# Optimization experiments

Measured on AMD Instinct MI355X. Metric: run time of the kernel, lower is better.

## Reference

```python
import jax, jax.numpy as jnp
import numpy as np

B, S, D, H = 2, 48, 256, 8
DH = D // H  # depth per head = 32
N = S * S    # flattened pair sequence length = 2304


def setup_inputs() -> dict:
    key = jax.random.key(0)
    ks = jax.random.split(key, 9)
    std = 1.0 / np.sqrt(D)
    x = jax.random.normal(ks[0], (B, S, S, D), dtype=jnp.float32)
    Wq = jax.random.normal(ks[1], (D, D), dtype=jnp.float32) * std
    Wk = jax.random.normal(ks[2], (D, D), dtype=jnp.float32) * std
    Wv = jax.random.normal(ks[3], (D, D), dtype=jnp.float32) * std
    Wo = jax.random.normal(ks[4], (D, D), dtype=jnp.float32) * std
    bq = jnp.zeros((D,), jnp.float32)
    bk = jnp.zeros((D,), jnp.float32)
    bv = jnp.zeros((D,), jnp.float32)
    bo = jnp.zeros((D,), jnp.float32)
    return {"pair_representation": x, "Wq": Wq, "bq": bq, "Wk": Wk, "bk": bk,
            "Wv": Wv, "bv": bv, "Wo": Wo, "bo": bo}


def reference(pair_representation, Wq, bq, Wk, bk, Wv, bv, Wo, bo):
    x = pair_representation.reshape(B, N, D)  # flatten (S,S) -> N

    def heads(t):  # (B,N,D) -> (B,H,N,DH)
        return t.reshape(B, N, H, DH).transpose(0, 2, 1, 3)

    q = heads(x @ Wq + bq)
    k = heads(x @ Wk + bk)
    v = heads(x @ Wv + bv)

    scale = 1.0 / jnp.sqrt(jnp.asarray(DH, jnp.float32))
    logits = jnp.einsum('bhnd,bhmd->bhnm', q, k) * scale  # (B,H,N,N)
    attn = jax.nn.softmax(logits, axis=-1)
    ctx = jnp.einsum('bhnm,bhmd->bhnd', attn, v)
    ctx = ctx.transpose(0, 2, 1, 3).reshape(B, N, D)
    return ctx @ Wo + bo  # (B, N, D)
```

## Files before the change

### kernel.cpp

```cpp
#include <hip/hip_runtime.h>
#include <math.h>

#define B 2
#define S 48
#define D 256
#define H 8
#define DH 32
#define N (S*S)
#define BN (B*N)
#define BH (B*H)
#define KS 6
#define KPZ (N/KS)
#define NE ((size_t)BN*D)
#define BHN (BH*N)

typedef _Float16 half8 __attribute__((ext_vector_type(8)));
typedef _Float16 half4_t __attribute__((ext_vector_type(4)));
typedef unsigned short ushort8_t __attribute__((ext_vector_type(8)));
typedef float floatx4 __attribute__((ext_vector_type(4)));

__device__ __forceinline__ void split8(const float* v, half8* hi, half8* lo) {
    #pragma unroll
    for (int j = 0; j < 8; j++) {
        _Float16 h = (_Float16)v[j];
        (*hi)[j] = h;
        (*lo)[j] = (_Float16)(v[j] - (float)h);
    }
}

__global__ __launch_bounds__(256) void proj_kernel(
    const float* __restrict__ x,
    const float* __restrict__ Wq, const float* __restrict__ bq,
    const float* __restrict__ Wk, const float* __restrict__ bk,
    const float* __restrict__ Wv, const float* __restrict__ bv,
    _Float16* __restrict__ qbuf, _Float16* __restrict__ kbuf,
    _Float16* __restrict__ vtbuf)
{
    __shared__ __align__(16) _Float16 BhS[64 * 72];
    __shared__ __align__(16) _Float16 BlS[64 * 72];

    const int z = blockIdx.z;
    const float* W    = (z == 0) ? Wq : (z == 1) ? Wk : Wv;
    const float* bias = (z == 0) ? bq : (z == 1) ? bk : bv;
    const float scale = (z == 0) ? rsqrtf((float)DH) * 1.44269504f : 1.0f;

    const int t = threadIdx.x;
    const int wv2 = t >> 6, lane = t & 63, l15 = lane & 15, quad = lane >> 4;
    const int rowb = blockIdx.x * 64;
    const int colb = blockIdx.y * 64;
    const int grow = rowb + wv2 * 16 + l15;
    floatx4 acc[4] = {{0,0,0,0},{0,0,0,0},{0,0,0,0},{0,0,0,0}};

    for (int kb0 = 0; kb0 < D; kb0 += 64) {
        __syncthreads();
        #pragma unroll
        for (int i = 0; i < 2; i++) {
            int u = i * 256 + t;
            int cc = u & 63, k0 = (u >> 6) * 8;
            float v[8];
            #pragma unroll
            for (int j = 0; j < 8; j++)
                v[j] = W[(size_t)(kb0 + k0 + j) * D + colb + cc];
            half8 hi, lo;
            split8(v, &hi, &lo);
            *(half8*)(BhS + cc * 72 + k0) = hi;
            *(half8*)(BlS + cc * 72 + k0) = lo;
        }
        __syncthreads();
        #pragma unroll
        for (int ksx = 0; ksx < 2; ksx++) {
            const float* xp = x + (size_t)grow * D + kb0 + ksx * 32 + quad * 8;
            float4 x0 = *(const float4*)xp;
            float4 x1 = *(const float4*)(xp + 4);
            float v[8] = {x0.x, x0.y, x0.z, x0.w, x1.x, x1.y, x1.z, x1.w};
            half8 ah, al;
            split8(v, &ah, &al);
            #pragma unroll
            for (int cg = 0; cg < 4; cg++) {
                half8 bh8 = *(const half8*)(BhS + (cg * 16 + l15) * 72 + ksx * 32 + quad * 8);
                half8 bl8 = *(const half8*)(BlS + (cg * 16 + l15) * 72 + ksx * 32 + quad * 8);
                acc[cg] = __builtin_amdgcn_mfma_f32_16x16x32_f16(ah, bh8, acc[cg], 0, 0, 0);
                acc[cg] = __builtin_amdgcn_mfma_f32_16x16x32_f16(al, bh8, acc[cg], 0, 0, 0);
                acc[cg] = __builtin_amdgcn_mfma_f32_16x16x32_f16(ah, bl8, acc[cg], 0, 0, 0);
            }
        }
    }

    const int bb = (rowb >= N) ? 1 : 0;
    #pragma unroll
    for (int cg = 0; cg < 4; cg++) {
        int col = colb + cg * 16 + l15;
        int hh = col >> 5, dh = col & 31;
        float bs = bias[col];
        if (z < 2) {
            _Float16* op = (z == 0) ? qbuf : kbuf;
            #pragma unroll
            for (int r = 0; r < 4; r++) {
                int n = rowb + wv2 * 16 + quad * 4 + r - bb * N;
                float v = (acc[cg][r] + bs) * scale;
                op[((size_t)(bb * H + hh) * N + n) * DH + dh] = (_Float16)v;
            }
        } else {
            int n0 = rowb + wv2 * 16 + quad * 4 - bb * N;
            half4_t pk;
            #pragma unroll
            for (int r = 0; r < 4; r++) pk[r] = (_Float16)(acc[cg][r] + bs);
            *(half4_t*)(vtbuf + ((size_t)(bb * H + hh) * DH + dh) * N + n0) = pk;
        }
    }
}

__global__ __launch_bounds__(256) void attn_kernel(
    const _Float16* __restrict__ qbuf, const _Float16* __restrict__ kbuf,
    const _Float16* __restrict__ vtbuf,
    _Float16* __restrict__ ctx_part, float* __restrict__ lpart)
{
    __shared__ __align__(16) _Float16 Ks[64 * 40];
    __shared__ __align__(16) _Float16 Vt[32 * 72];

    const int t = threadIdx.x;
    const int wv2 = t >> 6, lane = t & 63, l15 = lane & 15, quad = lane >> 4;
    const int bh = blockIdx.y, kz = blockIdx.z;
    const int qbase = blockIdx.x * 128 + wv2 * 32;

    half8 bq8[2];
    #pragma unroll
    for (int qg = 0; qg < 2; qg++)
        bq8[qg] = *(const half8*)(qbuf +
            ((size_t)bh * N + qbase + qg * 16 + l15) * DH + quad * 8);

    floatx4 acc[2][2] = {{{0,0,0,0},{0,0,0,0}},{{0,0,0,0},{0,0,0,0}}};
    float lsum[2] = {0.f, 0.f};

    const int skey = t >> 2, sd0 = (t & 3) * 8;
    const int svd = t >> 3, svk = (t & 7) * 8;

    for (int it = 0; it < KPZ / 64; it++) {
        const int key0 = kz * KPZ + it * 64;
        __syncthreads();
        *(ushort8_t*)(Ks + skey * 40 + sd0) =
            *(const ushort8_t*)(kbuf + ((size_t)bh * N + key0 + skey) * DH + sd0);
        *(ushort8_t*)(Vt + svd * 72 + svk) =
            *(const ushort8_t*)(vtbuf + ((size_t)bh * DH + svd) * N + key0 + svk);
        __syncthreads();

        #pragma unroll
        for (int kg = 0; kg < 4; kg++) {
            half8 ka = *(const half8*)(Ks + (kg * 16 + l15) * 40 + quad * 8);
            half4_t va0 = *(const half4_t*)(Vt + l15 * 72 + kg * 16 + quad * 4);
            half4_t va1 = *(const half4_t*)(Vt + (16 + l15) * 72 + kg * 16 + quad * 4);
            #pragma unroll
            for (int qg = 0; qg < 2; qg++) {
                floatx4 s = {0, 0, 0, 0};
                s = __builtin_amdgcn_mfma_f32_16x16x32_f16(ka, bq8[qg], s, 0, 0, 0);
                half4_t pf;
                #pragma unroll
                for (int r = 0; r < 4; r++) {
                    float p = exp2f(s[r]);
                    lsum[qg] += p;
                    pf[r] = (_Float16)p;
                }
                acc[qg][0] = __builtin_amdgcn_mfma_f32_16x16x16f16(va0, pf, acc[qg][0], 0, 0, 0);
                acc[qg][1] = __builtin_amdgcn_mfma_f32_16x16x16f16(va1, pf, acc[qg][1], 0, 0, 0);
            }
        }
    }

    const int bb = bh >> 3, hh = bh & 7;
    #pragma unroll
    for (int qg = 0; qg < 2; qg++) {
        float ls = lsum[qg];
        ls += __shfl_xor(ls, 16);
        ls += __shfl_xor(ls, 32);
        int q = qbase + qg * 16 + l15;
        if (quad == 0) lpart[(size_t)kz * BHN + bh * N + q] = ls;
        _Float16* crow = ctx_part + (size_t)kz * NE + ((size_t)bb * N + q) * D + hh * DH;
        half4_t c0, c1;
        #pragma unroll
        for (int r = 0; r < 4; r++) {
            c0[r] = (_Float16)acc[qg][0][r];
            c1[r] = (_Float16)acc[qg][1][r];
        }
        *(half4_t*)(crow + quad * 4)      = c0;
        *(half4_t*)(crow + 16 + quad * 4) = c1;
    }
}

__global__ __launch_bounds__(256) void outproj_kernel(
    const _Float16* __restrict__ ctx_part, const float* __restrict__ lpart,
    const float* __restrict__ Wo, const float* __restrict__ bo,
    float* __restrict__ out)
{
    __shared__ __align__(16) _Float16 BhS[64 * 72];
    __shared__ __align__(16) _Float16 BlS[64 * 72];
    __shared__ float Linv[64 * 8];

    const int t = threadIdx.x;
    const int wv2 = t >> 6, lane = t & 63, l15 = lane & 15, quad = lane >> 4;
    const int rowb = blockIdx.x * 64;
    const int colb = blockIdx.y * 64;
    const int grow = rowb + wv2 * 16 + l15;

    #pragma unroll
    for (int i = 0; i < 2; i++) {
        int idx = i * 256 + t;
        int r = idx >> 3, hh = idx & 7;
        int row = rowb + r;
        int bb = (row >= N) ? 1 : 0;
        int bhn = (bb * H + hh) * N + (row - bb * N);
        float ls = 0.f;
        #pragma unroll
        for (int zz = 0; zz < KS; zz++) ls += lpart[(size_t)zz * BHN + bhn];
        Linv[idx] = 1.0f / ls;
    }

    floatx4 acc[4] = {{0,0,0,0},{0,0,0,0},{0,0,0,0},{0,0,0,0}};

    for (int kb0 = 0; kb0 < D; kb0 += 64) {
        __syncthreads();
        #pragma unroll
        for (int i = 0; i < 2; i++) {
            int u = i * 256 + t;
            int cc = u & 63, k0 = (u >> 6) * 8;
            float v[8];
            #pragma unroll
            for (int j = 0; j < 8; j++)
                v[j] = Wo[(size_t)(kb0 + k0 + j) * D + colb + cc];
            half8 hi, lo;
            split8(v, &hi, &lo);
            *(half8*)(BhS + cc * 72 + k0) = hi;
            *(half8*)(BlS + cc * 72 + k0) = lo;
        }
        __syncthreads();
        #pragma unroll
        for (int ksx = 0; ksx < 2; ksx++) {
            const int kcol = kb0 + ksx * 32 + quad * 8;
            float linv = Linv[(wv2 * 16 + l15) * 8 + (kcol >> 5)];
            float v[8] = {};
            #pragma unroll
            for (int zz = 0; zz < KS; zz++) {
                half8 h = *(const half8*)(ctx_part + (size_t)zz * NE + (size_t)grow * D + kcol);
                #pragma unroll
                for (int j = 0; j < 8; j++) v[j] += (float)h[j];
            }
            #pragma unroll
            for (int j = 0; j < 8; j++) v[j] *= linv;
            half8 ah, al;
            split8(v, &ah, &al);
            #pragma unroll
            for (int cg = 0; cg < 4; cg++) {
                half8 bh8 = *(const half8*)(BhS + (cg * 16 + l15) * 72 + ksx * 32 + quad * 8);
                half8 bl8 = *(const half8*)(BlS + (cg * 16 + l15) * 72 + ksx * 32 + quad * 8);
                acc[cg] = __builtin_amdgcn_mfma_f32_16x16x32_f16(ah, bh8, acc[cg], 0, 0, 0);
                acc[cg] = __builtin_amdgcn_mfma_f32_16x16x32_f16(al, bh8, acc[cg], 0, 0, 0);
                acc[cg] = __builtin_amdgcn_mfma_f32_16x16x32_f16(ah, bl8, acc[cg], 0, 0, 0);
            }
        }
    }

    #pragma unroll
    for (int cg = 0; cg < 4; cg++) {
        int col = colb + cg * 16 + l15;
        float bs = bo[col];
        #pragma unroll
        for (int r = 0; r < 4; r++) {
            int row = rowb + wv2 * 16 + quad * 4 + r;
            out[(size_t)row * D + col] = acc[cg][r] + bs;
        }
    }
}

extern "C" void kernel_launch(void* const* d_in, const int* in_sizes, int n_in,
                              void* d_out, int out_size, void* d_ws, size_t ws_size,
                              hipStream_t stream)
{
    const float* x  = (const float*)d_in[0];
    const float* Wq = (const float*)d_in[1];
    const float* bq = (const float*)d_in[2];
    const float* Wk = (const float*)d_in[3];
    const float* bk = (const float*)d_in[4];
    const float* Wv = (const float*)d_in[5];
    const float* bv = (const float*)d_in[6];
    const float* Wo = (const float*)d_in[7];
    const float* bo = (const float*)d_in[8];
    float* out = (float*)d_out;

    _Float16* ctx_part = (_Float16*)d_ws;
    float* lpart    = (float*)(ctx_part + (size_t)KS * NE);
    _Float16* qbuf  = (_Float16*)(lpart + (size_t)KS * BHN);
    _Float16* kbuf  = qbuf + NE;
    _Float16* vtbuf = kbuf + NE;

    proj_kernel<<<dim3(BN / 64, D / 64, 3), 256, 0, stream>>>(
        x, Wq, bq, Wk, bk, Wv, bv, qbuf, kbuf, vtbuf);

    attn_kernel<<<dim3(N / 128, BH, KS), 256, 0, stream>>>(
        qbuf, kbuf, vtbuf, ctx_part, lpart);

    outproj_kernel<<<dim3(BN / 64, D / 64), 256, 0, stream>>>(
        ctx_part, lpart, Wo, bo, out);
}
```

Measured before the change: 133.9 us.

## Fuse projection, attention and output projection into one persistent kernel with grid barriers

Replaces three kernel launches with a single persistent kernel of 432 blocks that loops over the work items of each phase and separates phases with atomic-counter grid barriers. The aim is to remove launch overhead and inter-kernel gaps. In exchange it adds a memset, barrier spin costs, and a possible deadlock if all 432 blocks are not co-resident. The attention phase now runs fewer concurrent blocks than the original 1728-block grid, and the output phase uses only 288 of the blocks.

```diff
diff --git a/kernel.cpp b/kernel.cpp
--- a/kernel.cpp
+++ b/kernel.cpp
@@ -13,6 +13,7 @@
 #define KPZ (N/KS)
 #define NE ((size_t)BN*D)
 #define BHN (BH*N)
+#define GRID 432
 
 typedef _Float16 half8 __attribute__((ext_vector_type(8)));
 typedef _Float16 half4_t __attribute__((ext_vector_type(4)));
@@ -28,244 +29,256 @@
     }
 }
 
-__global__ __launch_bounds__(256) void proj_kernel(
+__device__ __forceinline__ void grid_barrier(unsigned* cnt) {
+    __threadfence();
+    __syncthreads();
+    if (threadIdx.x == 0) {
+        __hip_atomic_fetch_add(cnt, 1u, __ATOMIC_ACQ_REL, __HIP_MEMORY_SCOPE_AGENT);
+        long guard = 0;
+        while (__hip_atomic_load(cnt, __ATOMIC_ACQUIRE, __HIP_MEMORY_SCOPE_AGENT) < GRID
+               && ++guard < (1L << 31)) { }
+    }
+    __syncthreads();
+    __threadfence();
+}
+
+__global__ __launch_bounds__(256, 2) void fused_kernel(
     const float* __restrict__ x,
     const float* __restrict__ Wq, const float* __restrict__ bq,
     const float* __restrict__ Wk, const float* __restrict__ bk,
     const float* __restrict__ Wv, const float* __restrict__ bv,
+    const float* __restrict__ Wo, const float* __restrict__ bo,
+    float* __restrict__ out,
+    unsigned* __restrict__ counters,
+    _Float16* __restrict__ ctx_part, float* __restrict__ lpart,
     _Float16* __restrict__ qbuf, _Float16* __restrict__ kbuf,
     _Float16* __restrict__ vtbuf)
 {
-    __shared__ __align__(16) _Float16 BhS[64 * 72];
-    __shared__ __align__(16) _Float16 BlS[64 * 72];
-
-    const int z = blockIdx.z;
-    const float* W    = (z == 0) ? Wq : (z == 1) ? Wk : Wv;
-    const float* bias = (z == 0) ? bq : (z == 1) ? bk : bv;
-    const float scale = (z == 0) ? rsqrtf((float)DH) * 1.44269504f : 1.0f;
+    __shared__ __align__(16) unsigned char smem[20480];
 
     const int t = threadIdx.x;
+    const int bid = blockIdx.x;
     const int wv2 = t >> 6, lane = t & 63, l15 = lane & 15, quad = lane >> 4;
-    const int rowb = blockIdx.x * 64;
-    const int colb = blockIdx.y * 64;
-    const int grow = rowb + wv2 * 16 + l15;
-    floatx4 acc[4] = {{0,0,0,0},{0,0,0,0},{0,0,0,0},{0,0,0,0}};
-
-    for (int kb0 = 0; kb0 < D; kb0 += 64) {
-        __syncthreads();
+
+    {
+        _Float16* BhS = (_Float16*)smem;
+        _Float16* BlS = BhS + 64 * 72;
+        for (int u = bid; u < 864; u += GRID) {
+            const int z = u / 288, rem = u % 288;
+            const int rowb = (rem >> 2) * 64, colb = (rem & 3) * 64;
+            const float* W    = (z == 0) ? Wq : (z == 1) ? Wk : Wv;
+            const float* bias = (z == 0) ? bq : (z == 1) ? bk : bv;
+            const float scale = (z == 0) ? rsqrtf((float)DH) * 1.44269504f : 1.0f;
+            const int grow = rowb + wv2 * 16 + l15;
+            floatx4 acc[4] = {{0,0,0,0},{0,0,0,0},{0,0,0,0},{0,0,0,0}};
+
+            for (int kb0 = 0; kb0 < D; kb0 += 64) {
+                __syncthreads();
+                #pragma unroll
+                for (int i = 0; i < 2; i++) {
+                    int uu = i * 256 + t;
+                    int cc = uu & 63, k0 = (uu >> 6) * 8;
+                    float v[8];
+                    #pragma unroll
+                    for (int j = 0; j < 8; j++)
+                        v[j] = W[(size_t)(kb0 + k0 + j) * D + colb + cc];
+                    half8 hi, lo;
+                    split8(v, &hi, &lo);
+                    *(half8*)(BhS + cc * 72 + k0) = hi;
+                    *(half8*)(BlS + cc * 72 + k0) = lo;
+                }
+                __syncthreads();
+                #pragma unroll
+                for (int ksx = 0; ksx < 2; ksx++) {
+                    const float* xp = x + (size_t)grow * D + kb0 + ksx * 32 + quad * 8;
+                    float4 x0 = *(const float4*)xp;
+                    float4 x1 = *(const float4*)(xp + 4);
+                    float v[8] = {x0.x, x0.y, x0.z, x0.w, x1.x, x1.y, x1.z, x1.w};
+                    half8 ah, al;
+                    split8(v, &ah, &al);
+                    #pragma unroll
+                    for (int cg = 0; cg < 4; cg++) {
+                        half8 bh8 = *(const half8*)(BhS + (cg * 16 + l15) * 72 + ksx * 32 + quad * 8);
+                        half8 bl8 = *(const half8*)(BlS + (cg * 16 + l15) * 72 + ksx * 32 + quad * 8);
+                        acc[cg] = __builtin_amdgcn_mfma_f32_16x16x32_f16(ah, bh8, acc[cg], 0, 0, 0);
+                        acc[cg] = __builtin_amdgcn_mfma_f32_16x16x32_f16(al, bh8, acc[cg], 0, 0, 0);
+                        acc[cg] = __builtin_amdgcn_mfma_f32_16x16x32_f16(ah, bl8, acc[cg], 0, 0, 0);
+                    }
+                }
+            }
+
+            const int bb = (rowb >= N) ? 1 : 0;
+            #pragma unroll
+            for (int cg = 0; cg < 4; cg++) {
+                int col = colb + cg * 16 + l15;
+                int hh = col >> 5, dh = col & 31;
+                float bs = bias[col];
+                if (z < 2) {
+                    _Float16* op = (z == 0) ? qbuf : kbuf;
+                    #pragma unroll
+                    for (int r = 0; r < 4; r++) {
+                        int n = rowb + wv2 * 16 + quad * 4 + r - bb * N;
+                        float v = (acc[cg][r] + bs) * scale;
+                        op[((size_t)(bb * H + hh) * N + n) * DH + dh] = (_Float16)v;
+                    }
+                } else {
+                    int n0 = rowb + wv2 * 16 + quad * 4 - bb * N;
+                    half4_t pk;
+                    #pragma unroll
+                    for (int r = 0; r < 4; r++) pk[r] = (_Float16)(acc[cg][r] + bs);
+                    *(half4_t*)(vtbuf + ((size_t)(bb * H + hh) * DH + dh) * N + n0) = pk;
+                }
+            }
+        }
+    }
+    grid_barrier(&counters[0]);
+
+    {
+        _Float16* Ks = (_Float16*)smem;
+        _Float16* Vt = Ks + 64 * 40;
+        const int skey = t >> 2, sd0 = (t & 3) * 8;
+        const int svd = t >> 3, svk = (t & 7) * 8;
+
+        for (int u = bid; u < 1728; u += GRID) {
+            const int xq = u / 96, rem = u % 96;
+            const int bh = rem / 6, kz = rem % 6;
+            const int qbase = xq * 128 + wv2 * 32;
+
+            half8 bq8[2];
+            #pragma unroll
+            for (int qg = 0; qg < 2; qg++)
+                bq8[qg] = *(const half8*)(qbuf +
+                    ((size_t)bh * N + qbase + qg * 16 + l15) * DH + quad * 8);
+
+            floatx4 acc[2][2] = {{{0,0,0,0},{0,0,0,0}},{{0,0,0,0},{0,0,0,0}}};
+            float lsum[2] = {0.f, 0.f};
+
+            for (int it = 0; it < KPZ / 64; it++) {
+                const int key0 = kz * KPZ + it * 64;
+                __syncthreads();
+                *(ushort8_t*)(Ks + skey * 40 + sd0) =
+                    *(const ushort8_t*)(kbuf + ((size_t)bh * N + key0 + skey) * DH + sd0);
+                *(ushort8_t*)(Vt + svd * 72 + svk) =
+                    *(const ushort8_t*)(vtbuf + ((size_t)bh * DH + svd) * N + key0 + svk);
+                __syncthreads();
+
+                #pragma unroll
+                for (int kg = 0; kg < 4; kg++) {
+                    half8 ka = *(const half8*)(Ks + (kg * 16 + l15) * 40 + quad * 8);
+                    half4_t va0 = *(const half4_t*)(Vt + l15 * 72 + kg * 16 + quad * 4);
+                    half4_t va1 = *(const half4_t*)(Vt + (16 + l15) * 72 + kg * 16 + quad * 4);
+                    #pragma unroll
+                    for (int qg = 0; qg < 2; qg++) {
+                        floatx4 s = {0, 0, 0, 0};
+                        s = __builtin_amdgcn_mfma_f32_16x16x32_f16(ka, bq8[qg], s, 0, 0, 0);
+                        half4_t pf;
+                        #pragma unroll
+                        for (int r = 0; r < 4; r++) {
+                            float p = exp2f(s[r]);
+                            lsum[qg] += p;
+                            pf[r] = (_Float16)p;
+                        }
+                        acc[qg][0] = __builtin_amdgcn_mfma_f32_16x16x16f16(va0, pf, acc[qg][0], 0, 0, 0);
+                        acc[qg][1] = __builtin_amdgcn_mfma_f32_16x16x16f16(va1, pf, acc[qg][1], 0, 0, 0);
+                    }
+                }
+            }
+
+            const int bb = bh >> 3, hh = bh & 7;
+            #pragma unroll
+            for (int qg = 0; qg < 2; qg++) {
+                float ls = lsum[qg];
+                ls += __shfl_xor(ls, 16);
+                ls += __shfl_xor(ls, 32);
+                int q = qbase + qg * 16 + l15;
+                if (quad == 0) lpart[(size_t)kz * BHN + bh * N + q] = ls;
+                _Float16* crow = ctx_part + (size_t)kz * NE + ((size_t)bb * N + q) * D + hh * DH;
+                half4_t c0, c1;
+                #pragma unroll
+                for (int r = 0; r < 4; r++) {
+                    c0[r] = (_Float16)acc[qg][0][r];
+                    c1[r] = (_Float16)acc[qg][1][r];
+                }
+                *(half4_t*)(crow + quad * 4)      = c0;
+                *(half4_t*)(crow + 16 + quad * 4) = c1;
+            }
+        }
+    }
+    grid_barrier(&counters[1]);
+
+    if (bid < 288) {
+        _Float16* BhS = (_Float16*)smem;
+        _Float16* BlS = BhS + 64 * 72;
+        float* Linv = (float*)(smem + 18432);
+        const int rowb = (bid >> 2) * 64, colb = (bid & 3) * 64;
+        const int grow = rowb + wv2 * 16 + l15;
+
         #pragma unroll
         for (int i = 0; i < 2; i++) {
-            int u = i * 256 + t;
-            int cc = u & 63, k0 = (u >> 6) * 8;
-            float v[8];
-            #pragma unroll
-            for (int j = 0; j < 8; j++)
-                v[j] = W[(size_t)(kb0 + k0 + j) * D + colb + cc];
-            half8 hi, lo;
-            split8(v, &hi, &lo);
-            *(half8*)(BhS + cc * 72 + k0) = hi;
-            *(half8*)(BlS + cc * 72 + k0) = lo;
-        }
-        __syncthreads();
+            int idx = i * 256 + t;
+            int r = idx >> 3, hh = idx & 7;
+            int row = rowb + r;
+            int bb = (row >= N) ? 1 : 0;
+            int bhn = (bb * H + hh) * N + (row - bb * N);
+            float ls = 0.f;
+            #pragma unroll
+            for (int zz = 0; zz < KS; zz++) ls += lpart[(size_t)zz * BHN + bhn];
+            Linv[idx] = 1.0f / ls;
+        }
+
+        floatx4 acc[4] = {{0,0,0,0},{0,0,0,0},{0,0,0,0},{0,0,0,0}};
+
+        for (int kb0 = 0; kb0 < D; kb0 += 64) {
+            __syncthreads();
+            #pragma unroll
+            for (int i = 0; i < 2; i++) {
+                int uu = i * 256 + t;
+                int cc = uu & 63, k0 = (uu >> 6) * 8;
+                float v[8];
+                #pragma unroll
+                for (int j = 0; j < 8; j++)
+                    v[j] = Wo[(size_t)(kb0 + k0 + j) * D + colb + cc];
+                half8 hi, lo;
+                split8(v, &hi, &lo);
+                *(half8*)(BhS + cc * 72 + k0) = hi;
+                *(half8*)(BlS + cc * 72 + k0) = lo;
+            }
+            __syncthreads();
+            #pragma unroll
+            for (int ksx = 0; ksx < 2; ksx++) {
+                const int kcol = kb0 + ksx * 32 + quad * 8;
+                float linv = Linv[(wv2 * 16 + l15) * 8 + (kcol >> 5)];
+                float v[8] = {};
+                #pragma unroll
+                for (int zz = 0; zz < KS; zz++) {
+                    half8 h = *(const half8*)(ctx_part + (size_t)zz * NE + (size_t)grow * D + kcol);
+                    #pragma unroll
+                    for (int j = 0; j < 8; j++) v[j] += (float)h[j];
+                }
+                #pragma unroll
+                for (int j = 0; j < 8; j++) v[j] *= linv;
+                half8 ah, al;
+                split8(v, &ah, &al);
+                #pragma unroll
+                for (int cg = 0; cg < 4; cg++) {
+                    half8 bh8 = *(const half8*)(BhS + (cg * 16 + l15) * 72 + ksx * 32 + quad * 8);
+                    half8 bl8 = *(const half8*)(BlS + (cg * 16 + l15) * 72 + ksx * 32 + quad * 8);
+                    acc[cg] = __builtin_amdgcn_mfma_f32_16x16x32_f16(ah, bh8, acc[cg], 0, 0, 0);
+                    acc[cg] = __builtin_amdgcn_mfma_f32_16x16x32_f16(al, bh8, acc[cg], 0, 0, 0);
+                    acc[cg] = __builtin_amdgcn_mfma_f32_16x16x32_f16(ah, bl8, acc[cg], 0, 0, 0);
+                }
+            }
+        }
+
         #pragma unroll
-        for (int ksx = 0; ksx < 2; ksx++) {
-            const float* xp = x + (size_t)grow * D + kb0 + ksx * 32 + quad * 8;
-            float4 x0 = *(const float4*)xp;
-            float4 x1 = *(const float4*)(xp + 4);
-            float v[8] = {x0.x, x0.y, x0.z, x0.w, x1.x, x1.y, x1.z, x1.w};
-            half8 ah, al;
-            split8(v, &ah, &al);
-            #pragma unroll
-            for (int cg = 0; cg < 4; cg++) {
-                half8 bh8 = *(const half8*)(BhS + (cg * 16 + l15) * 72 + ksx * 32 + quad * 8);
-                half8 bl8 = *(const half8*)(BlS + (cg * 16 + l15) * 72 + ksx * 32 + quad * 8);
-                acc[cg] = __builtin_amdgcn_mfma_f32_16x16x32_f16(ah, bh8, acc[cg], 0, 0, 0);
-                acc[cg] = __builtin_amdgcn_mfma_f32_16x16x32_f16(al, bh8, acc[cg], 0, 0, 0);
-                acc[cg] = __builtin_amdgcn_mfma_f32_16x16x32_f16(ah, bl8, acc[cg], 0, 0, 0);
-            }
-        }
-    }
-
-    const int bb = (rowb >= N) ? 1 : 0;
-    #pragma unroll
-    for (int cg = 0; cg < 4; cg++) {
-        int col = colb + cg * 16 + l15;
-        int hh = col >> 5, dh = col & 31;
-        float bs = bias[col];
-        if (z < 2) {
-            _Float16* op = (z == 0) ? qbuf : kbuf;
+        for (int cg = 0; cg < 4; cg++) {
+            int col = colb + cg * 16 + l15;
+            float bs = bo[col];
             #pragma unroll
             for (int r = 0; r < 4; r++) {
-                int n = rowb + wv2 * 16 + quad * 4 + r - bb * N;
-                float v = (acc[cg][r] + bs) * scale;
-                op[((size_t)(bb * H + hh) * N + n) * DH + dh] = (_Float16)v;
-            }
-        } else {
-            int n0 = rowb + wv2 * 16 + quad * 4 - bb * N;
-            half4_t pk;
-            #pragma unroll
-            for (int r = 0; r < 4; r++) pk[r] = (_Float16)(acc[cg][r] + bs);
-            *(half4_t*)(vtbuf + ((size_t)(bb * H + hh) * DH + dh) * N + n0) = pk;
-        }
-    }
-}
-
-__global__ __launch_bounds__(256) void attn_kernel(
-    const _Float16* __restrict__ qbuf, const _Float16* __restrict__ kbuf,
-    const _Float16* __restrict__ vtbuf,
-    _Float16* __restrict__ ctx_part, float* __restrict__ lpart)
-{
-    __shared__ __align__(16) _Float16 Ks[64 * 40];
-    __shared__ __align__(16) _Float16 Vt[32 * 72];
-
-    const int t = threadIdx.x;
-    const int wv2 = t >> 6, lane = t & 63, l15 = lane & 15, quad = lane >> 4;
-    const int bh = blockIdx.y, kz = blockIdx.z;
-    const int qbase = blockIdx.x * 128 + wv2 * 32;
-
-    half8 bq8[2];
-    #pragma unroll
-    for (int qg = 0; qg < 2; qg++)
-        bq8[qg] = *(const half8*)(qbuf +
-            ((size_t)bh * N + qbase + qg * 16 + l15) * DH + quad * 8);
-
-    floatx4 acc[2][2] = {{{0,0,0,0},{0,0,0,0}},{{0,0,0,0},{0,0,0,0}}};
-    float lsum[2] = {0.f, 0.f};
-
-    const int skey = t >> 2, sd0 = (t & 3) * 8;
-    const int svd = t >> 3, svk = (t & 7) * 8;
-
-    for (int it = 0; it < KPZ / 64; it++) {
-        const int key0 = kz * KPZ + it * 64;
-        __syncthreads();
-        *(ushort8_t*)(Ks + skey * 40 + sd0) =
-            *(const ushort8_t*)(kbuf + ((size_t)bh * N + key0 + skey) * DH + sd0);
-        *(ushort8_t*)(Vt + svd * 72 + svk) =
-            *(const ushort8_t*)(vtbuf + ((size_t)bh * DH + svd) * N + key0 + svk);
-        __syncthreads();
-
-        #pragma unroll
-        for (int kg = 0; kg < 4; kg++) {
-            half8 ka = *(const half8*)(Ks + (kg * 16 + l15) * 40 + quad * 8);
-            half4_t va0 = *(const half4_t*)(Vt + l15 * 72 + kg * 16 + quad * 4);
-            half4_t va1 = *(const half4_t*)(Vt + (16 + l15) * 72 + kg * 16 + quad * 4);
-            #pragma unroll
-            for (int qg = 0; qg < 2; qg++) {
-                floatx4 s = {0, 0, 0, 0};
-                s = __builtin_amdgcn_mfma_f32_16x16x32_f16(ka, bq8[qg], s, 0, 0, 0);
-                half4_t pf;
-                #pragma unroll
-                for (int r = 0; r < 4; r++) {
-                    float p = exp2f(s[r]);
-                    lsum[qg] += p;
-                    pf[r] = (_Float16)p;
-                }
-                acc[qg][0] = __builtin_amdgcn_mfma_f32_16x16x16f16(va0, pf, acc[qg][0], 0, 0, 0);
-                acc[qg][1] = __builtin_amdgcn_mfma_f32_16x16x16f16(va1, pf, acc[qg][1], 0, 0, 0);
-            }
-        }
-    }
-
-    const int bb = bh >> 3, hh = bh & 7;
-    #pragma unroll
-    for (int qg = 0; qg < 2; qg++) {
-        float ls = lsum[qg];
-        ls += __shfl_xor(ls, 16);
-        ls += __shfl_xor(ls, 32);
-        int q = qbase + qg * 16 + l15;
-        if (quad == 0) lpart[(size_t)kz * BHN + bh * N + q] = ls;
-        _Float16* crow = ctx_part + (size_t)kz * NE + ((size_t)bb * N + q) * D + hh * DH;
-        half4_t c0, c1;
-        #pragma unroll
-        for (int r = 0; r < 4; r++) {
-            c0[r] = (_Float16)acc[qg][0][r];
-            c1[r] = (_Float16)acc[qg][1][r];
-        }
-        *(half4_t*)(crow + quad * 4)      = c0;
-        *(half4_t*)(crow + 16 + quad * 4) = c1;
-    }
-}
-
-__global__ __launch_bounds__(256) void outproj_kernel(
-    const _Float16* __restrict__ ctx_part, const float* __restrict__ lpart,
-    const float* __restrict__ Wo, const float* __restrict__ bo,
-    float* __restrict__ out)
-{
-    __shared__ __align__(16) _Float16 BhS[64 * 72];
-    __shared__ __align__(16) _Float16 BlS[64 * 72];
-    __shared__ float Linv[64 * 8];
-
-    const int t = threadIdx.x;
-    const int wv2 = t >> 6, lane = t & 63, l15 = lane & 15, quad = lane >> 4;
-    const int rowb = blockIdx.x * 64;
-    const int colb = blockIdx.y * 64;
-    const int grow = rowb + wv2 * 16 + l15;
-
-    #pragma unroll
-    for (int i = 0; i < 2; i++) {
-        int idx = i * 256 + t;
-        int r = idx >> 3, hh = idx & 7;
-        int row = rowb + r;
-        int bb = (row >= N) ? 1 : 0;
-        int bhn = (bb * H + hh) * N + (row - bb * N);
-        float ls = 0.f;
-        #pragma unroll
-        for (int zz = 0; zz < KS; zz++) ls += lpart[(size_t)zz * BHN + bhn];
-        Linv[idx] = 1.0f / ls;
-    }
-
-    floatx4 acc[4] = {{0,0,0,0},{0,0,0,0},{0,0,0,0},{0,0,0,0}};
-
-    for (int kb0 = 0; kb0 < D; kb0 += 64) {
-        __syncthreads();
-        #pragma unroll
-        for (int i = 0; i < 2; i++) {
-            int u = i * 256 + t;
-            int cc = u & 63, k0 = (u >> 6) * 8;
-            float v[8];
-            #pragma unroll
-            for (int j = 0; j < 8; j++)
-                v[j] = Wo[(size_t)(kb0 + k0 + j) * D + colb + cc];
-            half8 hi, lo;
-            split8(v, &hi, &lo);
-            *(half8*)(BhS + cc * 72 + k0) = hi;
-            *(half8*)(BlS + cc * 72 + k0) = lo;
-        }
-        __syncthreads();
-        #pragma unroll
-        for (int ksx = 0; ksx < 2; ksx++) {
-            const int kcol = kb0 + ksx * 32 + quad * 8;
-            float linv = Linv[(wv2 * 16 + l15) * 8 + (kcol >> 5)];
-            float v[8] = {};
-            #pragma unroll
-            for (int zz = 0; zz < KS; zz++) {
-                half8 h = *(const half8*)(ctx_part + (size_t)zz * NE + (size_t)grow * D + kcol);
-                #pragma unroll
-                for (int j = 0; j < 8; j++) v[j] += (float)h[j];
-            }
-            #pragma unroll
-            for (int j = 0; j < 8; j++) v[j] *= linv;
-            half8 ah, al;
-            split8(v, &ah, &al);
-            #pragma unroll
-            for (int cg = 0; cg < 4; cg++) {
-                half8 bh8 = *(const half8*)(BhS + (cg * 16 + l15) * 72 + ksx * 32 + quad * 8);
-                half8 bl8 = *(const half8*)(BlS + (cg * 16 + l15) * 72 + ksx * 32 + quad * 8);
-                acc[cg] = __builtin_amdgcn_mfma_f32_16x16x32_f16(ah, bh8, acc[cg], 0, 0, 0);
-                acc[cg] = __builtin_amdgcn_mfma_f32_16x16x32_f16(al, bh8, acc[cg], 0, 0, 0);
-                acc[cg] = __builtin_amdgcn_mfma_f32_16x16x32_f16(ah, bl8, acc[cg], 0, 0, 0);
-            }
-        }
-    }
-
-    #pragma unroll
-    for (int cg = 0; cg < 4; cg++) {
-        int col = colb + cg * 16 + l15;
-        float bs = bo[col];
-        #pragma unroll
-        for (int r = 0; r < 4; r++) {
-            int row = rowb + wv2 * 16 + quad * 4 + r;
-            out[(size_t)row * D + col] = acc[cg][r] + bs;
+                int row = rowb + wv2 * 16 + quad * 4 + r;
+                out[(size_t)row * D + col] = acc[cg][r] + bs;
+            }
         }
     }
 }
@@ -285,18 +298,16 @@
     const float* bo = (const float*)d_in[8];
     float* out = (float*)d_out;
 
-    _Float16* ctx_part = (_Float16*)d_ws;
+    unsigned* counters = (unsigned*)d_ws;
+    _Float16* ctx_part = (_Float16*)((char*)d_ws + 64);
     float* lpart    = (float*)(ctx_part + (size_t)KS * NE);
     _Float16* qbuf  = (_Float16*)(lpart + (size_t)KS * BHN);
     _Float16* kbuf  = qbuf + NE;
     _Float16* vtbuf = kbuf + NE;
 
-    proj_kernel<<<dim3(BN / 64, D / 64, 3), 256, 0, stream>>>(
-        x, Wq, bq, Wk, bk, Wv, bv, qbuf, kbuf, vtbuf);
-
-    attn_kernel<<<dim3(N / 128, BH, KS), 256, 0, stream>>>(
-        qbuf, kbuf, vtbuf, ctx_part, lpart);
-
-    outproj_kernel<<<dim3(BN / 64, D / 64), 256, 0, stream>>>(
-        ctx_part, lpart, Wo, bo, out);
+    hipMemsetAsync(d_ws, 0, 64, stream);
+
+    fused_kernel<<<dim3(GRID), dim3(256), 0, stream>>>(
+        x, Wq, bq, Wk, bk, Wv, bv, Wo, bo, out,
+        counters, ctx_part, lpart, qbuf, kbuf, vtbuf);
 }
```

Measured after the change: 421.4 us. +214.8%, slower.
